# Kernel tuning notes

Hardware: AMD Instinct MI355X
Metric: run time of the kernel (lower is better)

Reference implementation:

```python
import jax, jax.numpy as jnp
import numpy as np

N_HEADS = 16
MAX_LEN = 1024


def setup_inputs() -> dict:
    key = jax.random.key(0)
    ks = jax.random.split(key, 6)
    B, T, C = 4, 1024, 1024
    scale = 0.02
    return {
        "x": jax.random.normal(ks[0], (B, T, C), dtype=jnp.float32),
        "qkv_w": jax.random.normal(ks[1], (3 * C, C), dtype=jnp.float32) * scale,
        "qkv_b": jax.random.normal(ks[2], (3 * C,), dtype=jnp.float32) * scale,
        "proj_w": jax.random.normal(ks[3], (C, C), dtype=jnp.float32) * scale,
        "proj_b": jax.random.normal(ks[4], (C,), dtype=jnp.float32) * scale,
        "rel_pos_emb": jax.random.normal(ks[5], (2 * MAX_LEN - 1, C), dtype=jnp.float32) * scale,
    }


def reference(x, qkv_w, qkv_b, proj_w, proj_b, rel_pos_emb):
    B, T, C = x.shape
    H = N_HEADS
    D = C // H
    # QKV projection: (B,T,3C) -> (3,B,H,T,D)
    qkv = (x @ qkv_w.T + qkv_b).reshape(B, T, 3, H, D)
    qkv = jnp.transpose(qkv, (2, 0, 3, 1, 4))
    q, k, v = qkv[0], qkv[1], qkv[2]
    # scores: (B,H,T,T)
    att = jnp.einsum("bhtd,bhsd->bhts", q, k) / np.sqrt(D).astype(np.float32)
    # Relative position bias: gather-then-sum == sum-then-gather over head_dim.
    # Pre-reduce table to (2*max_len-1, H) to avoid materializing (T,T,C).
    table = rel_pos_emb.reshape(2 * MAX_LEN - 1, H, D).sum(axis=-1)  # (2L-1, H)
    pos = jnp.arange(T)
    rel_idx = pos[:, None] - pos[None, :] + (MAX_LEN - 1)  # (T,T)
    bias = jnp.transpose(table[rel_idx], (2, 0, 1))  # (H,T,T)
    att = att + bias[None]
    # causal mask: positions j > i masked to -inf
    causal = pos[None, :] > pos[:, None]  # (T,T) True above diagonal
    att = jnp.where(causal[None, None], -jnp.inf, att)
    att = jax.nn.softmax(att, axis=-1)
    out = jnp.einsum("bhts,bhsd->bhtd", att, v)  # (B,H,T,D)
    out = jnp.transpose(out, (0, 2, 1, 3)).reshape(B, T, C)
    return out @ proj_w.T + proj_b
```

## Files before the change

### kernel.cpp

```cpp
#include <hip/hip_runtime.h>
#include <hip/hip_bf16.h>


typedef __bf16 bf16x8 __attribute__((ext_vector_type(8)));
typedef float f32x4 __attribute__((ext_vector_type(4)));

__device__ __forceinline__ float bf2f(unsigned short u) {
    return __uint_as_float(((unsigned)u) << 16);
}
__device__ __forceinline__ unsigned short f2bf(float f) {
    __hip_bfloat16 h = __float2bfloat16(f);
    return *reinterpret_cast<unsigned short*>(&h);
}

__global__ __launch_bounds__(256) void cvt3_f32_bf16(const float* __restrict__ x,
                                                     const float* __restrict__ w,
                                                     const float* __restrict__ pw,
                                                     unsigned short* __restrict__ xb,
                                                     unsigned short* __restrict__ wb,
                                                     unsigned short* __restrict__ pwb) {
    const int bid = blockIdx.x;
    const float* in;
    unsigned short* out;
    int base;
    if (bid < 4096)      { in = x;  out = xb;  base = bid * 1024; }
    else if (bid < 7168) { in = w;  out = wb;  base = (bid - 4096) * 1024; }
    else                 { in = pw; out = pwb; base = (bid - 7168) * 1024; }
    const int i = base + threadIdx.x * 4;
    float4 v = *(const float4*)(in + i);
    out[i]     = f2bf(v.x);
    out[i + 1] = f2bf(v.y);
    out[i + 2] = f2bf(v.z);
    out[i + 3] = f2bf(v.w);
}

__global__ __launch_bounds__(256) void table_reduce(const float* __restrict__ rel,
                                                    float* __restrict__ table) {
    const int p = blockIdx.x;
    const int tid = threadIdx.x, lane = tid & 63, wave = tid >> 6;
    const float* r = rel + (size_t)p * 1024;
    float s[4];
#pragma unroll
    for (int k = 0; k < 4; ++k) s[k] = r[tid + 256 * k];
#pragma unroll
    for (int k = 0; k < 4; ++k) {
        float v = s[k];
        for (int o = 32; o; o >>= 1) v += __shfl_xor(v, o, 64);
        if (lane == 0) table[p * 16 + wave + 4 * k] = v;
    }
}

template <int EPI>
__global__ __launch_bounds__(256) void gemm_bt(const unsigned short* __restrict__ A,
                                               const unsigned short* __restrict__ Bm,
                                               const float* __restrict__ bias,
                                               unsigned short* __restrict__ outb,
                                               float* __restrict__ outf,
                                               int M, int N, int K) {
    __shared__ __attribute__((aligned(16))) unsigned short As[128 * 40];
    __shared__ __attribute__((aligned(16))) unsigned short Bs[128 * 40];
    const int bm = blockIdx.x * 128, bn = blockIdx.y * 128;
    const int tid = threadIdx.x, lane = tid & 63, wave = tid >> 6;
    const int wr = wave & 1, wc = wave >> 1;
    const int quad = lane >> 4, lm = lane & 15;

    const int srow = tid >> 1;
    const int scol = (tid & 1) * 16;
    const unsigned short* Ap = A + (size_t)(bm + srow) * K + scol;
    const unsigned short* Bp = Bm + (size_t)(bn + srow) * K + scol;
    unsigned short* AsW = &As[srow * 40 + scol];
    unsigned short* BsW = &Bs[srow * 40 + scol];

    f32x4 acc[4][4];
#pragma unroll
    for (int r = 0; r < 4; ++r)
#pragma unroll
        for (int c = 0; c < 4; ++c) acc[r][c] = (f32x4){0.f, 0.f, 0.f, 0.f};

    int4 pa0 = *(const int4*)(Ap);
    int4 pa1 = *(const int4*)(Ap + 8);
    int4 pb0 = *(const int4*)(Bp);
    int4 pb1 = *(const int4*)(Bp + 8);

    for (int kk = 0; kk < K; kk += 32) {
        *(int4*)(AsW)     = pa0;
        *(int4*)(AsW + 8) = pa1;
        *(int4*)(BsW)     = pb0;
        *(int4*)(BsW + 8) = pb1;
        __syncthreads();

        if (kk + 32 < K) {
            pa0 = *(const int4*)(Ap + kk + 32);
            pa1 = *(const int4*)(Ap + kk + 40);
            pb0 = *(const int4*)(Bp + kk + 32);
            pb1 = *(const int4*)(Bp + kk + 40);
        }

        bf16x8 af[4], bfr[4];
#pragma unroll
        for (int r = 0; r < 4; ++r)
            af[r] = *(const bf16x8*)(&As[(64 * wr + 16 * r + lm) * 40 + quad * 8]);
#pragma unroll
        for (int c = 0; c < 4; ++c)
            bfr[c] = *(const bf16x8*)(&Bs[(64 * wc + 16 * c + lm) * 40 + quad * 8]);
#pragma unroll
        for (int r = 0; r < 4; ++r)
#pragma unroll
            for (int c = 0; c < 4; ++c)
                acc[r][c] = __builtin_amdgcn_mfma_f32_16x16x32_bf16(af[r], bfr[c], acc[r][c], 0, 0, 0);
        __syncthreads();
    }

#pragma unroll
    for (int r = 0; r < 4; ++r)
#pragma unroll
        for (int c = 0; c < 4; ++c)
#pragma unroll
            for (int i = 0; i < 4; ++i) {
                const int row = bm + 64 * wr + 16 * r + quad * 4 + i;
                const int col = bn + 64 * wc + 16 * c + lm;
                const float v = acc[r][c][i] + bias[col];
                if (EPI == 0) {
                    const int b = row >> 10, t = row & 1023;
                    const int s3 = col >> 10, rem = col & 1023;
                    const int h = rem >> 6, d = rem & 63;
                    const size_t base = (((size_t)s3 * 4 + b) * 16 + h) * 65536;
                    const size_t off = base + (s3 == 2 ? (size_t)d * 1024 + t
                                                       : (size_t)t * 64 + d);
                    outb[off] = f2bf(v);
                } else {
                    outf[(size_t)row * N + col] = v;
                }
            }
}

__global__ __launch_bounds__(512) void attn_mfma(const unsigned short* __restrict__ qkvb,
                                                 const float* __restrict__ table,
                                                 unsigned short* __restrict__ y) {
    const int bh = blockIdx.x, b = bh >> 4, h = bh & 15;
    const int qb = (7 - blockIdx.y) * 128;
    const int tid = threadIdx.x, lane = tid & 63, wave = tid >> 6;
    const int quad = lane >> 4, lm = lane & 15;

    __shared__ __attribute__((aligned(16))) unsigned short Ks[64][72];
    __shared__ __attribute__((aligned(16))) unsigned short Vs[64][72];
    __shared__ __attribute__((aligned(16))) unsigned short Ps[8][16][72];
    __shared__ float tb[1280];

    const unsigned short* Qg  = qkvb + ((size_t)(b)*16 + h) * 65536;
    const unsigned short* Kg  = qkvb + ((size_t)(4 + b)*16 + h) * 65536;
    const unsigned short* Vtg = qkvb + ((size_t)(8 + b)*16 + h) * 65536;

    const bf16x8 qf0 = *(const bf16x8*)(Qg + (size_t)(qb + wave * 16 + lm) * 64 + quad * 8);
    const bf16x8 qf1 = *(const bf16x8*)(Qg + (size_t)(qb + wave * 16 + lm) * 64 + 32 + quad * 8);

    const int tbn = qb + 255;
    for (int i = tid; i < tbn; i += 512) tb[i] = table[(896 + i) * 16 + h];

    f32x4 oacc[4];
#pragma unroll
    for (int nb = 0; nb < 4; ++nb) oacc[nb] = (f32x4){0.f, 0.f, 0.f, 0.f};
    float mi[4], li[4];
#pragma unroll
    for (int i = 0; i < 4; ++i) { mi[i] = -1e30f; li[i] = 0.f; }

    const int ktiles = qb / 64 + 2;
    for (int kt = 0; kt < ktiles; ++kt) {
        __syncthreads();
        {
            const int r0 = tid >> 3, c0 = (tid & 7) * 8;
            *(int4*)&Ks[r0][c0] = *(const int4*)(Kg + (size_t)(kt * 64 + r0) * 64 + c0);
            *(int4*)&Vs[r0][c0] = *(const int4*)(Vtg + (size_t)r0 * 1024 + kt * 64 + c0);
        }
        __syncthreads();

        f32x4 s[4];
#pragma unroll
        for (int nb = 0; nb < 4; ++nb) {
            bf16x8 k0 = *(const bf16x8*)(&Ks[nb * 16 + lm][quad * 8]);
            bf16x8 k1 = *(const bf16x8*)(&Ks[nb * 16 + lm][32 + quad * 8]);
            s[nb] = (f32x4){0.f, 0.f, 0.f, 0.f};
            s[nb] = __builtin_amdgcn_mfma_f32_16x16x32_bf16(qf0, k0, s[nb], 0, 0, 0);
            s[nb] = __builtin_amdgcn_mfma_f32_16x16x32_bf16(qf1, k1, s[nb], 0, 0, 0);
        }

        const int qrow0 = qb + wave * 16 + quad * 4;
        const int jbase = kt * 64 + lm;
#pragma unroll
        for (int nb = 0; nb < 4; ++nb)
#pragma unroll
            for (int i = 0; i < 4; ++i) {
                const int q = qrow0 + i, j = jbase + nb * 16;
                const float v = fmaf(s[nb][i], 0.125f, tb[q - j + 127]);
                s[nb][i] = (j <= q) ? v : -1e30f;
            }

        float mnew[4], al[4];
#pragma unroll
        for (int i = 0; i < 4; ++i) {
            float mx = fmaxf(fmaxf(s[0][i], s[1][i]), fmaxf(s[2][i], s[3][i]));
            mx = fmaxf(mx, __shfl_xor(mx, 1, 64));
            mx = fmaxf(mx, __shfl_xor(mx, 2, 64));
            mx = fmaxf(mx, __shfl_xor(mx, 4, 64));
            mx = fmaxf(mx, __shfl_xor(mx, 8, 64));
            mnew[i] = fmaxf(mi[i], mx);
            al[i] = __expf(mi[i] - mnew[i]);
            mi[i] = mnew[i];
        }
#pragma unroll
        for (int nb = 0; nb < 4; ++nb)
#pragma unroll
            for (int i = 0; i < 4; ++i) s[nb][i] = __expf(s[nb][i] - mnew[i]);
#pragma unroll
        for (int i = 0; i < 4; ++i) {
            float sm = (s[0][i] + s[1][i]) + (s[2][i] + s[3][i]);
            sm += __shfl_xor(sm, 1, 64);
            sm += __shfl_xor(sm, 2, 64);
            sm += __shfl_xor(sm, 4, 64);
            sm += __shfl_xor(sm, 8, 64);
            li[i] = li[i] * al[i] + sm;
        }

#pragma unroll
        for (int nb = 0; nb < 4; ++nb)
#pragma unroll
            for (int i = 0; i < 4; ++i)
                Ps[wave][quad * 4 + i][nb * 16 + lm] = f2bf(s[nb][i]);

#pragma unroll
        for (int nb = 0; nb < 4; ++nb)
#pragma unroll
            for (int i = 0; i < 4; ++i) oacc[nb][i] *= al[i];

        const bf16x8 p0 = *(const bf16x8*)(&Ps[wave][lm][quad * 8]);
        const bf16x8 p1 = *(const bf16x8*)(&Ps[wave][lm][32 + quad * 8]);
#pragma unroll
        for (int nb = 0; nb < 4; ++nb) {
            bf16x8 v0 = *(const bf16x8*)(&Vs[nb * 16 + lm][quad * 8]);
            bf16x8 v1 = *(const bf16x8*)(&Vs[nb * 16 + lm][32 + quad * 8]);
            oacc[nb] = __builtin_amdgcn_mfma_f32_16x16x32_bf16(p0, v0, oacc[nb], 0, 0, 0);
            oacc[nb] = __builtin_amdgcn_mfma_f32_16x16x32_bf16(p1, v1, oacc[nb], 0, 0, 0);
        }
    }

    float inv[4];
#pragma unroll
    for (int i = 0; i < 4; ++i) inv[i] = 1.0f / li[i];
#pragma unroll
    for (int nb = 0; nb < 4; ++nb)
#pragma unroll
        for (int i = 0; i < 4; ++i) {
            const int q = qb + wave * 16 + quad * 4 + i;
            const int d = nb * 16 + lm;
            y[((size_t)(b * 1024 + q)) * 1024 + h * 64 + d] = f2bf(oacc[nb][i] * inv[i]);
        }
}

extern "C" void kernel_launch(void* const* d_in, const int* in_sizes, int n_in,
                              void* d_out, int out_size, void* d_ws, size_t ws_size,
                              hipStream_t stream) {
    const float* x      = (const float*)d_in[0];
    const float* qkv_w  = (const float*)d_in[1];
    const float* qkv_b  = (const float*)d_in[2];
    const float* proj_w = (const float*)d_in[3];
    const float* proj_b = (const float*)d_in[4];
    const float* rel    = (const float*)d_in[5];
    float* out = (float*)d_out;

    char* ws = (char*)d_ws;
    unsigned short* xb   = (unsigned short*)(ws);
    unsigned short* wb   = (unsigned short*)(ws + 8388608);
    unsigned short* pwb  = (unsigned short*)(ws + 14680064);
    float* table         = (float*)(ws + 16777216);
    unsigned short* qkvb = (unsigned short*)(ws + 16908288);
    unsigned short* yb   = (unsigned short*)(ws + 42074112);

    cvt3_f32_bf16<<<8192, 256, 0, stream>>>(x, qkv_w, proj_w, xb, wb, pwb);
    table_reduce<<<2047, 256, 0, stream>>>(rel, table);
    gemm_bt<0><<<dim3(32, 24), 256, 0, stream>>>(xb, wb, qkv_b, qkvb, nullptr, 4096, 3072, 1024);
    attn_mfma<<<dim3(64, 8), 512, 0, stream>>>(qkvb, table, yb);
    gemm_bt<1><<<dim3(32, 8), 256, 0, stream>>>(yb, pwb, proj_b, nullptr, out, 4096, 1024, 1024);
}
```

Baseline: 219.2 us.

## Double-buffer GEMM shared memory tiles and merge prep kernels into one launch

The GEMM now uses two LDS buffers and two register staging slots. The next tile is written to the alternate buffer after the MFMAs, so each K-step needs one barrier instead of two and global loads are issued two steps ahead. The bf16 conversion kernel and the position-table reduction are merged into one launch to save a kernel launch. This doubles LDS use per block, which may lower occupancy, and the macro-based two-step unroll assumes K is a multiple of 64.

```diff
diff --git a/kernel.cpp b/kernel.cpp
--- a/kernel.cpp
+++ b/kernel.cpp
@@ -13,42 +13,71 @@
     return *reinterpret_cast<unsigned short*>(&h);
 }
 
-__global__ __launch_bounds__(256) void cvt3_f32_bf16(const float* __restrict__ x,
-                                                     const float* __restrict__ w,
-                                                     const float* __restrict__ pw,
-                                                     unsigned short* __restrict__ xb,
-                                                     unsigned short* __restrict__ wb,
-                                                     unsigned short* __restrict__ pwb) {
+__global__ __launch_bounds__(256) void prep(const float* __restrict__ x,
+                                            const float* __restrict__ w,
+                                            const float* __restrict__ pw,
+                                            const float* __restrict__ rel,
+                                            unsigned short* __restrict__ xb,
+                                            unsigned short* __restrict__ wb,
+                                            unsigned short* __restrict__ pwb,
+                                            float* __restrict__ table) {
     const int bid = blockIdx.x;
-    const float* in;
-    unsigned short* out;
-    int base;
-    if (bid < 4096)      { in = x;  out = xb;  base = bid * 1024; }
-    else if (bid < 7168) { in = w;  out = wb;  base = (bid - 4096) * 1024; }
-    else                 { in = pw; out = pwb; base = (bid - 7168) * 1024; }
-    const int i = base + threadIdx.x * 4;
-    float4 v = *(const float4*)(in + i);
-    out[i]     = f2bf(v.x);
-    out[i + 1] = f2bf(v.y);
-    out[i + 2] = f2bf(v.z);
-    out[i + 3] = f2bf(v.w);
-}
-
-__global__ __launch_bounds__(256) void table_reduce(const float* __restrict__ rel,
-                                                    float* __restrict__ table) {
-    const int p = blockIdx.x;
-    const int tid = threadIdx.x, lane = tid & 63, wave = tid >> 6;
-    const float* r = rel + (size_t)p * 1024;
-    float s[4];
-#pragma unroll
-    for (int k = 0; k < 4; ++k) s[k] = r[tid + 256 * k];
-#pragma unroll
-    for (int k = 0; k < 4; ++k) {
-        float v = s[k];
-        for (int o = 32; o; o >>= 1) v += __shfl_xor(v, o, 64);
-        if (lane == 0) table[p * 16 + wave + 4 * k] = v;
-    }
-}
+    const int tid = threadIdx.x;
+    if (bid < 8192) {
+        const float* in;
+        unsigned short* out;
+        int base;
+        if (bid < 4096)      { in = x;  out = xb;  base = bid * 1024; }
+        else if (bid < 7168) { in = w;  out = wb;  base = (bid - 4096) * 1024; }
+        else                 { in = pw; out = pwb; base = (bid - 7168) * 1024; }
+        const int i = base + tid * 4;
+        float4 v = *(const float4*)(in + i);
+        out[i]     = f2bf(v.x);
+        out[i + 1] = f2bf(v.y);
+        out[i + 2] = f2bf(v.z);
+        out[i + 3] = f2bf(v.w);
+    } else {
+        const int p = bid - 8192;
+        const int lane = tid & 63, wave = tid >> 6;
+        const float* r = rel + (size_t)p * 1024;
+        float s[4];
+#pragma unroll
+        for (int k = 0; k < 4; ++k) s[k] = r[tid + 256 * k];
+#pragma unroll
+        for (int k = 0; k < 4; ++k) {
+            float v = s[k];
+            for (int o = 32; o; o >>= 1) v += __shfl_xor(v, o, 64);
+            if (lane == 0) table[p * 16 + wave + 4 * k] = v;
+        }
+    }
+}
+
+
+#define GEMM_STEP(KK, WRS, LDSI, CB)                                                     \
+    {                                                                                    \
+        __syncthreads();                                                                 \
+        if ((KK) + 64 < K) {                                                             \
+            pa[LDSI][0] = *(const int4*)(Ap + (KK) + 64);                                \
+            pa[LDSI][1] = *(const int4*)(Ap + (KK) + 72);                                \
+            pb[LDSI][0] = *(const int4*)(Bp + (KK) + 64);                                \
+            pb[LDSI][1] = *(const int4*)(Bp + (KK) + 72);                                \
+        }                                                                                \
+        bf16x8 af[4], bfr[4];                                                            \
+        _Pragma("unroll") for (int r = 0; r < 4; ++r)                                    \
+            af[r] = *(const bf16x8*)(&As[CB][(64 * wr + 16 * r + lm) * 40 + quad * 8]);  \
+        _Pragma("unroll") for (int c = 0; c < 4; ++c)                                    \
+            bfr[c] = *(const bf16x8*)(&Bs[CB][(64 * wc + 16 * c + lm) * 40 + quad * 8]); \
+        _Pragma("unroll") for (int r = 0; r < 4; ++r)                                    \
+            _Pragma("unroll") for (int c = 0; c < 4; ++c)                                \
+                acc[r][c] = __builtin_amdgcn_mfma_f32_16x16x32_bf16(af[r], bfr[c],       \
+                                                                    acc[r][c], 0, 0, 0);\
+        if ((KK) + 32 < K) {                                                             \
+            *(int4*)(&As[(CB) ^ 1][woff])     = pa[WRS][0];                              \
+            *(int4*)(&As[(CB) ^ 1][woff] + 8) = pa[WRS][1];                              \
+            *(int4*)(&Bs[(CB) ^ 1][woff])     = pb[WRS][0];                              \
+            *(int4*)(&Bs[(CB) ^ 1][woff] + 8) = pb[WRS][1];                              \
+        }                                                                                \
+    }
 
 template <int EPI>
 __global__ __launch_bounds__(256) void gemm_bt(const unsigned short* __restrict__ A,
@@ -57,8 +86,8 @@
                                                unsigned short* __restrict__ outb,
                                                float* __restrict__ outf,
                                                int M, int N, int K) {
-    __shared__ __attribute__((aligned(16))) unsigned short As[128 * 40];
-    __shared__ __attribute__((aligned(16))) unsigned short Bs[128 * 40];
+    __shared__ __attribute__((aligned(16))) unsigned short As[2][128 * 40];
+    __shared__ __attribute__((aligned(16))) unsigned short Bs[2][128 * 40];
     const int bm = blockIdx.x * 128, bn = blockIdx.y * 128;
     const int tid = threadIdx.x, lane = tid & 63, wave = tid >> 6;
     const int wr = wave & 1, wc = wave >> 1;
@@ -68,8 +97,7 @@
     const int scol = (tid & 1) * 16;
     const unsigned short* Ap = A + (size_t)(bm + srow) * K + scol;
     const unsigned short* Bp = Bm + (size_t)(bn + srow) * K + scol;
-    unsigned short* AsW = &As[srow * 40 + scol];
-    unsigned short* BsW = &Bs[srow * 40 + scol];
+    const int woff = srow * 40 + scol;
 
     f32x4 acc[4][4];
 #pragma unroll
@@ -77,38 +105,23 @@
 #pragma unroll
         for (int c = 0; c < 4; ++c) acc[r][c] = (f32x4){0.f, 0.f, 0.f, 0.f};
 
-    int4 pa0 = *(const int4*)(Ap);
-    int4 pa1 = *(const int4*)(Ap + 8);
-    int4 pb0 = *(const int4*)(Bp);
-    int4 pb1 = *(const int4*)(Bp + 8);
-
-    for (int kk = 0; kk < K; kk += 32) {
-        *(int4*)(AsW)     = pa0;
-        *(int4*)(AsW + 8) = pa1;
-        *(int4*)(BsW)     = pb0;
-        *(int4*)(BsW + 8) = pb1;
-        __syncthreads();
-
-        if (kk + 32 < K) {
-            pa0 = *(const int4*)(Ap + kk + 32);
-            pa1 = *(const int4*)(Ap + kk + 40);
-            pb0 = *(const int4*)(Bp + kk + 32);
-            pb1 = *(const int4*)(Bp + kk + 40);
-        }
-
-        bf16x8 af[4], bfr[4];
-#pragma unroll
-        for (int r = 0; r < 4; ++r)
-            af[r] = *(const bf16x8*)(&As[(64 * wr + 16 * r + lm) * 40 + quad * 8]);
-#pragma unroll
-        for (int c = 0; c < 4; ++c)
-            bfr[c] = *(const bf16x8*)(&Bs[(64 * wc + 16 * c + lm) * 40 + quad * 8]);
-#pragma unroll
-        for (int r = 0; r < 4; ++r)
-#pragma unroll
-            for (int c = 0; c < 4; ++c)
-                acc[r][c] = __builtin_amdgcn_mfma_f32_16x16x32_bf16(af[r], bfr[c], acc[r][c], 0, 0, 0);
-        __syncthreads();
+    int4 pa[2][2], pb[2][2];
+    pa[0][0] = *(const int4*)(Ap);
+    pa[0][1] = *(const int4*)(Ap + 8);
+    pb[0][0] = *(const int4*)(Bp);
+    pb[0][1] = *(const int4*)(Bp + 8);
+    *(int4*)(&As[0][woff])     = pa[0][0];
+    *(int4*)(&As[0][woff] + 8) = pa[0][1];
+    *(int4*)(&Bs[0][woff])     = pb[0][0];
+    *(int4*)(&Bs[0][woff] + 8) = pb[0][1];
+    pa[1][0] = *(const int4*)(Ap + 32);
+    pa[1][1] = *(const int4*)(Ap + 40);
+    pb[1][0] = *(const int4*)(Bp + 32);
+    pb[1][1] = *(const int4*)(Bp + 40);
+
+    for (int kk = 0; kk < K; kk += 64) {
+        GEMM_STEP(kk,      1, 0, 0);
+        GEMM_STEP(kk + 32, 0, 1, 1);
     }
 
 #pragma unroll
@@ -275,8 +288,7 @@
     unsigned short* qkvb = (unsigned short*)(ws + 16908288);
     unsigned short* yb   = (unsigned short*)(ws + 42074112);
 
-    cvt3_f32_bf16<<<8192, 256, 0, stream>>>(x, qkv_w, proj_w, xb, wb, pwb);
-    table_reduce<<<2047, 256, 0, stream>>>(rel, table);
+    prep<<<10239, 256, 0, stream>>>(x, qkv_w, proj_w, rel, xb, wb, pwb, table);
     gemm_bt<0><<<dim3(32, 24), 256, 0, stream>>>(xb, wb, qkv_b, qkvb, nullptr, 4096, 3072, 1024);
     attn_mfma<<<dim3(64, 8), 512, 0, stream>>>(qkvb, table, yb);
     gemm_bt<1><<<dim3(32, 8), 256, 0, stream>>>(yb, pwb, proj_b, nullptr, out, 4096, 1024, 1024);
```

After: 312.8 us. +42.7%, slower.

## Fuse fp32-to-bf16 conversion into GEMM tile loads and use 8-wave blocks

Applied to the files above, without the earlier changes.

Removes the separate conversion kernel. The QKV GEMM now loads x and qkv_w directly as fp32 and converts them to bf16 while staging into shared memory. The projection GEMM likewise converts proj_w on the fly. Blocks grow to 512 threads, with each wave computing a 64x32 sub-tile instead of 64x64. This saves a kernel launch and the write and re-read of the bf16 copies, at the cost of twice the global/L2 bytes per tile load and repeated conversion work across blocks.

```diff
diff --git a/kernel.cpp b/kernel.cpp
--- a/kernel.cpp
+++ b/kernel.cpp
@@ -12,26 +12,11 @@
     __hip_bfloat16 h = __float2bfloat16(f);
     return *reinterpret_cast<unsigned short*>(&h);
 }
-
-__global__ __launch_bounds__(256) void cvt3_f32_bf16(const float* __restrict__ x,
-                                                     const float* __restrict__ w,
-                                                     const float* __restrict__ pw,
-                                                     unsigned short* __restrict__ xb,
-                                                     unsigned short* __restrict__ wb,
-                                                     unsigned short* __restrict__ pwb) {
-    const int bid = blockIdx.x;
-    const float* in;
-    unsigned short* out;
-    int base;
-    if (bid < 4096)      { in = x;  out = xb;  base = bid * 1024; }
-    else if (bid < 7168) { in = w;  out = wb;  base = (bid - 4096) * 1024; }
-    else                 { in = pw; out = pwb; base = (bid - 7168) * 1024; }
-    const int i = base + threadIdx.x * 4;
-    float4 v = *(const float4*)(in + i);
-    out[i]     = f2bf(v.x);
-    out[i + 1] = f2bf(v.y);
-    out[i + 2] = f2bf(v.z);
-    out[i + 3] = f2bf(v.w);
+__device__ __forceinline__ int4 cvt8(float4 a, float4 b) {
+    union { unsigned short s[8]; int4 v; } u;
+    u.s[0] = f2bf(a.x); u.s[1] = f2bf(a.y); u.s[2] = f2bf(a.z); u.s[3] = f2bf(a.w);
+    u.s[4] = f2bf(b.x); u.s[5] = f2bf(b.y); u.s[6] = f2bf(b.z); u.s[7] = f2bf(b.w);
+    return u.v;
 }
 
 __global__ __launch_bounds__(256) void table_reduce(const float* __restrict__ rel,
@@ -50,9 +35,9 @@
     }
 }
 
-template <int EPI>
-__global__ __launch_bounds__(256) void gemm_bt(const unsigned short* __restrict__ A,
-                                               const unsigned short* __restrict__ Bm,
+template <int EPI, bool AF32>
+__global__ __launch_bounds__(512) void gemm_bt(const void* __restrict__ Ain,
+                                               const float* __restrict__ Bf,
                                                const float* __restrict__ bias,
                                                unsigned short* __restrict__ outb,
                                                float* __restrict__ outf,
@@ -64,49 +49,58 @@
     const int wr = wave & 1, wc = wave >> 1;
     const int quad = lane >> 4, lm = lane & 15;
 
-    const int srow = tid >> 1;
-    const int scol = (tid & 1) * 16;
-    const unsigned short* Ap = A + (size_t)(bm + srow) * K + scol;
-    const unsigned short* Bp = Bm + (size_t)(bn + srow) * K + scol;
+    const int srow = tid >> 2;
+    const int scol = (tid & 3) * 8;
+    const float* ApF          = (const float*)Ain + (size_t)(bm + srow) * K + scol;
+    const unsigned short* ApH = (const unsigned short*)Ain + (size_t)(bm + srow) * K + scol;
+    const float* BpF          = Bf + (size_t)(bn + srow) * K + scol;
     unsigned short* AsW = &As[srow * 40 + scol];
     unsigned short* BsW = &Bs[srow * 40 + scol];
 
-    f32x4 acc[4][4];
+    f32x4 acc[4][2];
 #pragma unroll
     for (int r = 0; r < 4; ++r)
 #pragma unroll
-        for (int c = 0; c < 4; ++c) acc[r][c] = (f32x4){0.f, 0.f, 0.f, 0.f};
-
-    int4 pa0 = *(const int4*)(Ap);
-    int4 pa1 = *(const int4*)(Ap + 8);
-    int4 pb0 = *(const int4*)(Bp);
-    int4 pb1 = *(const int4*)(Bp + 8);
+        for (int c = 0; c < 2; ++c) acc[r][c] = (f32x4){0.f, 0.f, 0.f, 0.f};
+
+    float4 paf0, paf1, pbf0, pbf1;
+    int4 pah;
+    if (AF32) {
+        paf0 = *(const float4*)(ApF);
+        paf1 = *(const float4*)(ApF + 4);
+    } else {
+        pah = *(const int4*)(ApH);
+    }
+    pbf0 = *(const float4*)(BpF);
+    pbf1 = *(const float4*)(BpF + 4);
 
     for (int kk = 0; kk < K; kk += 32) {
-        *(int4*)(AsW)     = pa0;
-        *(int4*)(AsW + 8) = pa1;
-        *(int4*)(BsW)     = pb0;
-        *(int4*)(BsW + 8) = pb1;
+        *(int4*)(AsW) = AF32 ? cvt8(paf0, paf1) : pah;
+        *(int4*)(BsW) = cvt8(pbf0, pbf1);
         __syncthreads();
 
         if (kk + 32 < K) {
-            pa0 = *(const int4*)(Ap + kk + 32);
-            pa1 = *(const int4*)(Ap + kk + 40);
-            pb0 = *(const int4*)(Bp + kk + 32);
-            pb1 = *(const int4*)(Bp + kk + 40);
-        }
-
-        bf16x8 af[4], bfr[4];
+            if (AF32) {
+                paf0 = *(const float4*)(ApF + kk + 32);
+                paf1 = *(const float4*)(ApF + kk + 36);
+            } else {
+                pah = *(const int4*)(ApH + kk + 32);
+            }
+            pbf0 = *(const float4*)(BpF + kk + 32);
+            pbf1 = *(const float4*)(BpF + kk + 36);
+        }
+
+        bf16x8 af[4], bfr[2];
 #pragma unroll
         for (int r = 0; r < 4; ++r)
             af[r] = *(const bf16x8*)(&As[(64 * wr + 16 * r + lm) * 40 + quad * 8]);
 #pragma unroll
-        for (int c = 0; c < 4; ++c)
-            bfr[c] = *(const bf16x8*)(&Bs[(64 * wc + 16 * c + lm) * 40 + quad * 8]);
+        for (int c = 0; c < 2; ++c)
+            bfr[c] = *(const bf16x8*)(&Bs[(32 * wc + 16 * c + lm) * 40 + quad * 8]);
 #pragma unroll
         for (int r = 0; r < 4; ++r)
 #pragma unroll
-            for (int c = 0; c < 4; ++c)
+            for (int c = 0; c < 2; ++c)
                 acc[r][c] = __builtin_amdgcn_mfma_f32_16x16x32_bf16(af[r], bfr[c], acc[r][c], 0, 0, 0);
         __syncthreads();
     }
@@ -114,11 +108,11 @@
 #pragma unroll
     for (int r = 0; r < 4; ++r)
 #pragma unroll
-        for (int c = 0; c < 4; ++c)
+        for (int c = 0; c < 2; ++c)
 #pragma unroll
             for (int i = 0; i < 4; ++i) {
                 const int row = bm + 64 * wr + 16 * r + quad * 4 + i;
-                const int col = bn + 64 * wc + 16 * c + lm;
+                const int col = bn + 32 * wc + 16 * c + lm;
                 const float v = acc[r][c][i] + bias[col];
                 if (EPI == 0) {
                     const int b = row >> 10, t = row & 1023;
@@ -268,16 +262,14 @@
     float* out = (float*)d_out;
 
     char* ws = (char*)d_ws;
-    unsigned short* xb   = (unsigned short*)(ws);
-    unsigned short* wb   = (unsigned short*)(ws + 8388608);
-    unsigned short* pwb  = (unsigned short*)(ws + 14680064);
     float* table         = (float*)(ws + 16777216);
     unsigned short* qkvb = (unsigned short*)(ws + 16908288);
     unsigned short* yb   = (unsigned short*)(ws + 42074112);
 
-    cvt3_f32_bf16<<<8192, 256, 0, stream>>>(x, qkv_w, proj_w, xb, wb, pwb);
     table_reduce<<<2047, 256, 0, stream>>>(rel, table);
-    gemm_bt<0><<<dim3(32, 24), 256, 0, stream>>>(xb, wb, qkv_b, qkvb, nullptr, 4096, 3072, 1024);
+    gemm_bt<0, true><<<dim3(32, 24), 512, 0, stream>>>(x, qkv_w, qkv_b, qkvb, nullptr,
+                                                       4096, 3072, 1024);
     attn_mfma<<<dim3(64, 8), 512, 0, stream>>>(qkvb, table, yb);
-    gemm_bt<1><<<dim3(32, 8), 256, 0, stream>>>(yb, pwb, proj_b, nullptr, out, 4096, 1024, 1024);
-}
+    gemm_bt<1, false><<<dim3(32, 8), 512, 0, stream>>>(yb, proj_w, proj_b, nullptr, out,
+                                                       4096, 1024, 1024);
+}
```

Measured after the change: 205.6 us. 6.2% less time.
